# Kernel tuning notes

Measured on AMD Instinct MI355X. Metric: run time of the kernel, lower is better.

## Reference

```python
import jax, jax.numpy as jnp
from jax import lax
import numpy as np

B, L, IN_DIM = 1, 2048, 1024
D_MODEL, D_INNER, D_STATE, DT_RANK, D_CONV, N_LAYERS = 512, 1024, 16, 32, 4, 2


def _ln(x, w, b):
    m = jnp.mean(x, -1, keepdims=True)
    v = jnp.var(x, -1, keepdims=True)
    return (x - m) * lax.rsqrt(v + 1e-5) * w + b


def _rms(x, w):
    return x * lax.rsqrt(jnp.mean(x * x, -1, keepdims=True) + 1e-5) * w


def _assoc_scan(dA, dBx):
    # first-order linear recurrence h_t = dA_t * h_{t-1} + dBx_t via associative scan
    def comb(e1, e2):
        a1, b1 = e1
        a2, b2 = e2
        return a1 * a2, a2 * b1 + b2
    return lax.associative_scan(comb, (dA, dBx), axis=1)[1]


def _mamba_layer(h, in_w, cw, cb, xw, dtw, dtb, alog, Dp, ow, rw):
    hn = _rms(h, rw)                              # pre-norm (RMSNorm)
    xz = hn @ in_w                                # [b,l,2*d_inner]
    xi, z = jnp.split(xz, 2, -1)
    # causal depthwise conv1d (kernel d_conv, left pad d_conv-1)
    xc = lax.conv_general_dilated(xi.transpose(0, 2, 1), cw, (1,), [(D_CONV - 1, 0)],
                                  feature_group_count=D_INNER,
                                  dimension_numbers=('NCH', 'OIH', 'NCH')) + cb[None, :, None]
    xi = jax.nn.silu(xc.transpose(0, 2, 1))       # [b,l,d_inner]
    dbc = xi @ xw                                 # [b,l,dt_rank+2*d_state]
    dt, Bm, Cm = jnp.split(dbc, [DT_RANK, DT_RANK + D_STATE], -1)
    delta = jax.nn.softplus(dt @ dtw + dtb)       # [b,l,d_inner]
    A = -jnp.exp(alog)                            # [d_inner, d_state]
    dA = jnp.exp(delta[..., None] * A)            # [b,l,d_inner,d_state]
    dBx = (delta * xi)[..., None] * Bm[:, :, None, :]
    hs = _assoc_scan(dA, dBx)                     # [b,l,d_inner,d_state]
    y = jnp.einsum('bldn,bln->bld', hs, Cm) + xi * Dp
    y = y * jax.nn.silu(z)
    return h + y @ ow


def _conv_t(x, w, b, s, p):
    # PyTorch ConvTranspose2d, weight layout [Cin, Cout, k, k]
    kT = jnp.flip(w, (2, 3)).transpose(1, 0, 2, 3)
    pad = w.shape[2] - 1 - p
    y = lax.conv_general_dilated(x, kT, (1, 1), [(pad, pad), (pad, pad)],
                                 lhs_dilation=(s, s),
                                 dimension_numbers=('NCHW', 'OIHW', 'NCHW'))
    return y + b[None, :, None, None]


def _fwd(x, coords, W_fc1, b_fc1, W_pos, b_pos,
         mamba_in_w, mamba_conv_w, mamba_conv_b, mamba_x_w, mamba_dt_w, mamba_dt_b,
         mamba_A_log, mamba_D, mamba_out_w, mamba_rms_w,
         ln_w, ln_b, Wa1, ba1, Wa2, ba2,
         ct1_w, ct1_b, ct2_w, ct2_b, ct3_w, ct3_b, ct4_w, ct4_b, ct5_w, ct5_b):
    h = jax.nn.gelu(x @ W_fc1 + b_fc1, approximate=False)   # _fc1
    h = h + (coords @ W_pos + b_pos)[None]                  # linear pos-emb
    for l in range(N_LAYERS):
        h = _mamba_layer(h, mamba_in_w[l], mamba_conv_w[l], mamba_conv_b[l],
                         mamba_x_w[l], mamba_dt_w[l], mamba_dt_b[l],
                         mamba_A_log[l], mamba_D[l], mamba_out_w[l], mamba_rms_w[l])
    h = _ln(h, ln_w, ln_b)
    A = jnp.tanh(h @ Wa1 + ba1) @ Wa2 + ba2                 # [1,L,1]
    A = jax.nn.softmax(A.transpose(0, 2, 1), axis=-1)       # [1,1,L]
    pooled = jnp.einsum('bol,bld->bod', A, h)               # [1,1,512]
    feat = pooled.reshape(x.shape[0], D_MODEL, 1, 1)
    y = jax.nn.relu(_conv_t(feat, ct1_w, ct1_b, 1, 0))      # 1 -> 4
    y = jax.nn.relu(_conv_t(y, ct2_w, ct2_b, 4, 0))         # 4 -> 16
    y = jax.nn.relu(_conv_t(y, ct3_w, ct3_b, 2, 1))         # 16 -> 32
    y = jax.nn.relu(_conv_t(y, ct4_w, ct4_b, 2, 1))         # 32 -> 64
    return _conv_t(y, ct5_w, ct5_b, 2, 1)                   # 64 -> 128, 11 classes


def setup_inputs() -> dict:
    key = jax.random.key(0)
    ks = jax.random.split(key, 32)
    n = lambda k, s, sc=0.02: jax.random.normal(k, s, jnp.float32) * sc
    inp = {
        'x': jax.random.normal(ks[0], (B, L, IN_DIM), jnp.float32),
        'coords': jax.random.uniform(ks[1], (L, 2), jnp.float32),
        'W_fc1': n(ks[2], (IN_DIM, D_MODEL)), 'b_fc1': jnp.zeros((D_MODEL,)),
        'W_pos': n(ks[3], (2, D_MODEL)), 'b_pos': jnp.zeros((D_MODEL,)),
        'mamba_in_w': n(ks[4], (N_LAYERS, D_MODEL, 2 * D_INNER)),
        'mamba_conv_w': n(ks[5], (N_LAYERS, D_INNER, 1, D_CONV), 0.1),
        'mamba_conv_b': jnp.zeros((N_LAYERS, D_INNER)),
        'mamba_x_w': n(ks[6], (N_LAYERS, D_INNER, DT_RANK + 2 * D_STATE)),
        'mamba_dt_w': n(ks[7], (N_LAYERS, DT_RANK, D_INNER), 0.1),
        'mamba_dt_b': jnp.full((N_LAYERS, D_INNER), -4.0, jnp.float32),
        'mamba_A_log': jnp.tile(jnp.log(jnp.arange(1, D_STATE + 1, dtype=jnp.float32)), (N_LAYERS, D_INNER, 1)),
        'mamba_D': jnp.ones((N_LAYERS, D_INNER), jnp.float32),
        'mamba_out_w': n(ks[8], (N_LAYERS, D_INNER, D_MODEL)),
        'mamba_rms_w': jnp.ones((N_LAYERS, D_MODEL), jnp.float32),
        'ln_w': jnp.ones((D_MODEL,)), 'ln_b': jnp.zeros((D_MODEL,)),
        'Wa1': n(ks[9], (D_MODEL, 128)), 'ba1': jnp.zeros((128,)),
        'Wa2': n(ks[10], (128, 1)), 'ba2': jnp.zeros((1,)),
        'ct1_w': n(ks[11], (512, 256, 4, 4)), 'ct1_b': jnp.zeros((256,)),
        'ct2_w': n(ks[12], (256, 128, 4, 4)), 'ct2_b': jnp.zeros((128,)),
        'ct3_w': n(ks[13], (128, 64, 4, 4)), 'ct3_b': jnp.zeros((64,)),
        'ct4_w': n(ks[14], (64, 32, 4, 4)), 'ct4_b': jnp.zeros((32,)),
        'ct5_w': n(ks[15], (32, 11, 4, 4)), 'ct5_b': jnp.zeros((11,)),
    }
    return inp


def reference(x, coords, W_fc1, b_fc1, W_pos, b_pos,
              mamba_in_w, mamba_conv_w, mamba_conv_b, mamba_x_w, mamba_dt_w, mamba_dt_b,
              mamba_A_log, mamba_D, mamba_out_w, mamba_rms_w,
              ln_w, ln_b, Wa1, ba1, Wa2, ba2,
              ct1_w, ct1_b, ct2_w, ct2_b, ct3_w, ct3_b, ct4_w, ct4_b, ct5_w, ct5_b):
    return _fwd(x, coords, W_fc1, b_fc1, W_pos, b_pos,
                mamba_in_w, mamba_conv_w, mamba_conv_b, mamba_x_w, mamba_dt_w, mamba_dt_b,
                mamba_A_log, mamba_D, mamba_out_w, mamba_rms_w,
                ln_w, ln_b, Wa1, ba1, Wa2, ba2,
                ct1_w, ct1_b, ct2_w, ct2_b, ct3_w, ct3_b, ct4_w, ct4_b, ct5_w, ct5_b)
```

## Files before the change

### kernel.cpp

```cpp
#include <hip/hip_runtime.h>
#include <math.h>

#define LSEQ 2048
#define DM 512
#define DI 1024
#define NST 16
#define CHUNK 128
#define NC (LSEQ / CHUNK)

__device__ __forceinline__ float siluf(float v) { return v / (1.f + expf(-v)); }

__global__ __launch_bounds__(256) void gemm_mt(
    const float* __restrict__ A, int lda,
    const float* __restrict__ B, int ldb,
    float* __restrict__ out, int ldc, int Ktot)
{
    __shared__ float As[16][68];
    __shared__ float Bs[16][132];
    const int tid = threadIdx.x;
    const int tx = tid & 15, ty = tid >> 4;
    const int n0 = blockIdx.x << 7, m0 = blockIdx.y << 6;
    const int z = blockIdx.z, nz = gridDim.z;
    const int Kz = Ktot / nz, kb = z * Kz;
    const int arow = tid >> 2, ak = (tid & 3) << 2;
    const int bkr = tid >> 5, bcol = (tid & 31) << 2;
    const float* Ap = A + (size_t)(m0 + arow) * lda + kb + ak;
    const float* Bp = B + (size_t)(kb + bkr) * ldb + n0 + bcol;
    float acc[4][8] = {};
    float4 av = *(const float4*)(Ap);
    float4 bv0 = *(const float4*)(Bp);
    float4 bv1 = *(const float4*)(Bp + (size_t)8 * ldb);
    for (int k0 = 0; k0 < Kz; k0 += 16) {
        As[ak + 0][arow] = av.x;
        As[ak + 1][arow] = av.y;
        As[ak + 2][arow] = av.z;
        As[ak + 3][arow] = av.w;
        *(float4*)&Bs[bkr][bcol] = bv0;
        *(float4*)&Bs[bkr + 8][bcol] = bv1;
        __syncthreads();
        if (k0 + 16 < Kz) {
            av = *(const float4*)(Ap + k0 + 16);
            bv0 = *(const float4*)(Bp + (size_t)(k0 + 16) * ldb);
            bv1 = *(const float4*)(Bp + (size_t)(k0 + 24) * ldb);
        }
#pragma unroll
        for (int kk = 0; kk < 16; ++kk) {
            float4 a = *(const float4*)&As[kk][ty << 2];
            float4 b0 = *(const float4*)&Bs[kk][tx << 2];
            float4 b1 = *(const float4*)&Bs[kk][(tx << 2) + 64];
            float a4[4] = {a.x, a.y, a.z, a.w};
            float b8[8] = {b0.x, b0.y, b0.z, b0.w, b1.x, b1.y, b1.z, b1.w};
#pragma unroll
            for (int i = 0; i < 4; ++i)
#pragma unroll
                for (int j = 0; j < 8; ++j)
                    acc[i][j] = fmaf(a4[i], b8[j], acc[i][j]);
        }
        __syncthreads();
    }
    const int Mtot = gridDim.y << 6;
    float* op = out + (size_t)z * Mtot * ldc;
#pragma unroll
    for (int i = 0; i < 4; ++i) {
        float* Cp = op + (size_t)(m0 + (ty << 2) + i) * ldc + n0 + (tx << 2);
        *(float4*)Cp = make_float4(acc[i][0], acc[i][1], acc[i][2], acc[i][3]);
        *(float4*)(Cp + 64) = make_float4(acc[i][4], acc[i][5], acc[i][6], acc[i][7]);
    }
}

__global__ __launch_bounds__(256) void sk_reduce(
    const float* __restrict__ part, float* __restrict__ out, int S, int nz, int add)
{
    const int idx = blockIdx.x * 256 + threadIdx.x;
    if (idx >= S) return;
    float s = 0.f;
    for (int zz = 0; zz < nz; ++zz) s += part[(size_t)zz * S + idx];
    if (add) out[idx] += s; else out[idx] = s;
}

__global__ __launch_bounds__(256) void gemm64(
    const float* __restrict__ A, int lda,
    const float* __restrict__ B, int ldb,
    float* __restrict__ C, int ldc,
    int K, int accum)
{
    __shared__ float As[16][68];
    __shared__ float Bs[16][68];
    const int tid = threadIdx.x;
    const int tx = tid & 15, ty = tid >> 4;
    const int m0 = blockIdx.y << 6, n0 = blockIdx.x << 6;
    const int arow = tid >> 2, akk = (tid & 3) << 2;
    const int bkr = tid >> 4, bnn = (tid & 15) << 2;
    const float* Ap = A + (size_t)(m0 + arow) * lda + akk;
    const float* Bp = B + (size_t)bkr * ldb + n0 + bnn;
    float acc[4][4] = {};
    for (int k0 = 0; k0 < K; k0 += 16) {
        float4 av = *(const float4*)(Ap + k0);
        float4 bv = *(const float4*)(Bp + (size_t)k0 * ldb);
        As[akk + 0][arow] = av.x;
        As[akk + 1][arow] = av.y;
        As[akk + 2][arow] = av.z;
        As[akk + 3][arow] = av.w;
        *(float4*)&Bs[bkr][bnn] = bv;
        __syncthreads();
#pragma unroll
        for (int kk = 0; kk < 16; ++kk) {
            float4 a = *(const float4*)&As[kk][ty << 2];
            float4 b = *(const float4*)&Bs[kk][tx << 2];
            acc[0][0] = fmaf(a.x, b.x, acc[0][0]);
            acc[0][1] = fmaf(a.x, b.y, acc[0][1]);
            acc[0][2] = fmaf(a.x, b.z, acc[0][2]);
            acc[0][3] = fmaf(a.x, b.w, acc[0][3]);
            acc[1][0] = fmaf(a.y, b.x, acc[1][0]);
            acc[1][1] = fmaf(a.y, b.y, acc[1][1]);
            acc[1][2] = fmaf(a.y, b.z, acc[1][2]);
            acc[1][3] = fmaf(a.y, b.w, acc[1][3]);
            acc[2][0] = fmaf(a.z, b.x, acc[2][0]);
            acc[2][1] = fmaf(a.z, b.y, acc[2][1]);
            acc[2][2] = fmaf(a.z, b.z, acc[2][2]);
            acc[2][3] = fmaf(a.z, b.w, acc[2][3]);
            acc[3][0] = fmaf(a.w, b.x, acc[3][0]);
            acc[3][1] = fmaf(a.w, b.y, acc[3][1]);
            acc[3][2] = fmaf(a.w, b.z, acc[3][2]);
            acc[3][3] = fmaf(a.w, b.w, acc[3][3]);
        }
        __syncthreads();
    }
#pragma unroll
    for (int i = 0; i < 4; ++i) {
        float* Cp = C + (size_t)(m0 + (ty << 2) + i) * ldc + n0 + (tx << 2);
        if (accum) {
            Cp[0] += acc[i][0]; Cp[1] += acc[i][1]; Cp[2] += acc[i][2]; Cp[3] += acc[i][3];
        } else {
            Cp[0] = acc[i][0]; Cp[1] = acc[i][1]; Cp[2] = acc[i][2]; Cp[3] = acc[i][3];
        }
    }
}

__global__ __launch_bounds__(256) void xproj_splitk(
    const float* __restrict__ A, const float* __restrict__ B,
    float* __restrict__ part)
{
    __shared__ float As[16][68];
    __shared__ float Bs[16][68];
    const int tid = threadIdx.x;
    const int tx = tid & 15, ty = tid >> 4;
    const int ks = blockIdx.x;
    const int m0 = blockIdx.y << 6;
    const int arow = tid >> 2, ak = (tid & 3) << 2;
    const int bkr = tid >> 4, bcol = (tid & 15) << 2;
    const int kbase = ks << 7;
    const float* Ap = A + (size_t)(m0 + arow) * DI + kbase + ak;
    const float* Bp = B + (size_t)(kbase + bkr) * 64 + bcol;
    float acc[4][4] = {};
    for (int k0 = 0; k0 < 128; k0 += 16) {
        float4 av = *(const float4*)(Ap + k0);
        float4 bv = *(const float4*)(Bp + k0 * 64);
        As[ak + 0][arow] = av.x;
        As[ak + 1][arow] = av.y;
        As[ak + 2][arow] = av.z;
        As[ak + 3][arow] = av.w;
        *(float4*)&Bs[bkr][bcol] = bv;
        __syncthreads();
#pragma unroll
        for (int kk = 0; kk < 16; ++kk) {
            float4 a = *(const float4*)&As[kk][ty << 2];
            float4 b = *(const float4*)&Bs[kk][tx << 2];
            acc[0][0] = fmaf(a.x, b.x, acc[0][0]);
            acc[0][1] = fmaf(a.x, b.y, acc[0][1]);
            acc[0][2] = fmaf(a.x, b.z, acc[0][2]);
            acc[0][3] = fmaf(a.x, b.w, acc[0][3]);
            acc[1][0] = fmaf(a.y, b.x, acc[1][0]);
            acc[1][1] = fmaf(a.y, b.y, acc[1][1]);
            acc[1][2] = fmaf(a.y, b.z, acc[1][2]);
            acc[1][3] = fmaf(a.y, b.w, acc[1][3]);
            acc[2][0] = fmaf(a.z, b.x, acc[2][0]);
            acc[2][1] = fmaf(a.z, b.y, acc[2][1]);
            acc[2][2] = fmaf(a.z, b.z, acc[2][2]);
            acc[2][3] = fmaf(a.z, b.w, acc[2][3]);
            acc[3][0] = fmaf(a.w, b.x, acc[3][0]);
            acc[3][1] = fmaf(a.w, b.y, acc[3][1]);
            acc[3][2] = fmaf(a.w, b.z, acc[3][2]);
            acc[3][3] = fmaf(a.w, b.w, acc[3][3]);
        }
        __syncthreads();
    }
#pragma unroll
    for (int i = 0; i < 4; ++i) {
        float* Cp = part + ((size_t)ks * LSEQ + m0 + (ty << 2) + i) * 64 + (tx << 2);
        Cp[0] = acc[i][0]; Cp[1] = acc[i][1]; Cp[2] = acc[i][2]; Cp[3] = acc[i][3];
    }
}

__global__ __launch_bounds__(256) void xproj_reduce(
    const float* __restrict__ part, float* __restrict__ dbc)
{
    const int idx = blockIdx.x * 256 + threadIdx.x;
    float s = 0.f;
#pragma unroll
    for (int ks = 0; ks < 8; ++ks) s += part[(size_t)ks * LSEQ * 64 + idx];
    dbc[idx] = s;
}

__global__ __launch_bounds__(256) void fc1_epi(
    const float* __restrict__ tmp, const float* __restrict__ bfc1,
    const float* __restrict__ coords, const float* __restrict__ Wpos,
    const float* __restrict__ bpos, float* __restrict__ h)
{
    int idx = blockIdx.x * 256 + threadIdx.x;
    int t = idx >> 9, j = idx & 511;
    float v = tmp[idx] + bfc1[j];
    float g = 0.5f * v * (1.f + erff(v * 0.70710678118654752f));
    h[idx] = g + coords[2 * t] * Wpos[j] + coords[2 * t + 1] * Wpos[DM + j] + bpos[j];
}

__global__ __launch_bounds__(256) void rmsnorm_k(
    const float* __restrict__ h, const float* __restrict__ w, float* __restrict__ out)
{
    const int t = blockIdx.x, tid = threadIdx.x;
    float a = h[(size_t)t * DM + tid];
    float b = h[(size_t)t * DM + 256 + tid];
    float ss = a * a + b * b;
#pragma unroll
    for (int off = 1; off < 64; off <<= 1) ss += __shfl_xor(ss, off);
    __shared__ float red[4];
    if ((tid & 63) == 0) red[tid >> 6] = ss;
    __syncthreads();
    float tot = red[0] + red[1] + red[2] + red[3];
    float inv = rsqrtf(tot * (1.f / DM) + 1e-5f);
    out[(size_t)t * DM + tid] = a * inv * w[tid];
    out[(size_t)t * DM + 256 + tid] = b * inv * w[256 + tid];
}

__global__ __launch_bounds__(256) void layernorm_k(
    const float* __restrict__ h, const float* __restrict__ w,
    const float* __restrict__ bb, float* __restrict__ out)
{
    const int t = blockIdx.x, tid = threadIdx.x;
    float a = h[(size_t)t * DM + tid];
    float b = h[(size_t)t * DM + 256 + tid];
    float s = a + b;
#pragma unroll
    for (int off = 1; off < 64; off <<= 1) s += __shfl_xor(s, off);
    __shared__ float red1[4];
    if ((tid & 63) == 0) red1[tid >> 6] = s;
    __syncthreads();
    float mean = (red1[0] + red1[1] + red1[2] + red1[3]) * (1.f / DM);
    float da = a - mean, db = b - mean;
    float vs = da * da + db * db;
#pragma unroll
    for (int off = 1; off < 64; off <<= 1) vs += __shfl_xor(vs, off);
    __shared__ float red2[4];
    if ((tid & 63) == 0) red2[tid >> 6] = vs;
    __syncthreads();
    float var = (red2[0] + red2[1] + red2[2] + red2[3]) * (1.f / DM);
    float inv = rsqrtf(var + 1e-5f);
    out[(size_t)t * DM + tid] = da * inv * w[tid] + bb[tid];
    out[(size_t)t * DM + 256 + tid] = db * inv * w[256 + tid] + bb[256 + tid];
}

__global__ __launch_bounds__(256) void conv_silu_k(
    const float* __restrict__ xz, const float* __restrict__ cw,
    const float* __restrict__ cb, float* __restrict__ xc)
{
    int idx = blockIdx.x * 256 + threadIdx.x;
    int t = idx >> 10, c = idx & 1023;
    float w0 = cw[c * 4], w1 = cw[c * 4 + 1], w2 = cw[c * 4 + 2], w3 = cw[c * 4 + 3];
    float s = cb[c];
    if (t >= 3) s = fmaf(xz[(size_t)(t - 3) * 2048 + c], w0, s);
    if (t >= 2) s = fmaf(xz[(size_t)(t - 2) * 2048 + c], w1, s);
    if (t >= 1) s = fmaf(xz[(size_t)(t - 1) * 2048 + c], w2, s);
    s = fmaf(xz[(size_t)t * 2048 + c], w3, s);
    xc[idx] = siluf(s);
}

__global__ __launch_bounds__(256) void softplus_k(
    float* __restrict__ delta, const float* __restrict__ dtb)
{
    int idx = blockIdx.x * 256 + threadIdx.x;
    int d = idx & 1023;
    float v = delta[idx] + dtb[d];
    delta[idx] = fmaxf(v, 0.f) + log1pf(expf(-fabsf(v)));
}

__global__ __launch_bounds__(256) void scan_p1(
    const float* __restrict__ delta, const float* __restrict__ xc,
    const float* __restrict__ dbc, const float* __restrict__ alog,
    float* __restrict__ aprod, float* __restrict__ hfin)
{
    __shared__ float sD[CHUNK][16], sX[CHUNK][16], sB[CHUNK][16];
    const int tid = threadIdx.x;
    const int g = tid >> 4, n = tid & 15;
    const int d0 = blockIdx.x << 4;
    const int c = blockIdx.y;
    const int t0 = c * CHUNK;
    const int d = d0 + g;
    const float An = -expf(alog[d * NST + n]);
    for (int i = tid; i < CHUNK * 16; i += 256) {
        int r = i >> 4, cc = i & 15;
        sD[r][cc] = delta[(size_t)(t0 + r) * DI + d0 + cc];
        sX[r][cc] = xc[(size_t)(t0 + r) * DI + d0 + cc];
        sB[r][cc] = dbc[(size_t)(t0 + r) * 64 + 32 + cc];
    }
    __syncthreads();
    float h = 0.f, ap = 1.f;
    for (int i = 0; i < CHUNK; ++i) {
        float dl = sD[i][g], xv = sX[i][g];
        float a = expf(dl * An);
        h = fmaf(a, h, dl * xv * sB[i][n]);
        ap *= a;
    }
    size_t idx = ((size_t)c * DI + d) * NST + n;
    aprod[idx] = ap;
    hfin[idx] = h;
}

__global__ __launch_bounds__(256) void scan_carry(
    const float* __restrict__ aprod, const float* __restrict__ hfin,
    float* __restrict__ carry)
{
    const int dn = blockIdx.x * 256 + threadIdx.x;
    float h = 0.f;
    carry[dn] = 0.f;
#pragma unroll
    for (int c = 0; c < NC - 1; ++c) {
        h = fmaf(aprod[(size_t)c * DI * NST + dn], h, hfin[(size_t)c * DI * NST + dn]);
        carry[(size_t)(c + 1) * DI * NST + dn] = h;
    }
}

__global__ __launch_bounds__(256) void scan_p2(
    const float* __restrict__ delta, const float* __restrict__ xc,
    const float* __restrict__ dbc, const float* __restrict__ xz,
    const float* __restrict__ alog, const float* __restrict__ Dp,
    const float* __restrict__ carry, float* __restrict__ y)
{
    __shared__ float sD[CHUNK][16], sX[CHUNK][16], sB[CHUNK][16], sC[CHUNK][16], sZ[CHUNK][16];
    const int tid = threadIdx.x;
    const int g = tid >> 4, n = tid & 15;
    const int d0 = blockIdx.x << 4;
    const int c = blockIdx.y;
    const int t0 = c * CHUNK;
    const int d = d0 + g;
    const float An = -expf(alog[d * NST + n]);
    const float Dd = Dp[d];
    for (int i = tid; i < CHUNK * 16; i += 256) {
        int r = i >> 4, cc = i & 15;
        sD[r][cc] = delta[(size_t)(t0 + r) * DI + d0 + cc];
        sX[r][cc] = xc[(size_t)(t0 + r) * DI + d0 + cc];
        sB[r][cc] = dbc[(size_t)(t0 + r) * 64 + 32 + cc];
        sC[r][cc] = dbc[(size_t)(t0 + r) * 64 + 48 + cc];
        sZ[r][cc] = xz[(size_t)(t0 + r) * 2048 + 1024 + d0 + cc];
    }
    __syncthreads();
    float h = carry[((size_t)c * DI + d) * NST + n];
    for (int i = 0; i < CHUNK; ++i) {
        float dl = sD[i][g], xv = sX[i][g];
        float a = expf(dl * An);
        h = fmaf(a, h, dl * xv * sB[i][n]);
        float p = h * sC[i][n];
        p += __shfl_xor(p, 1, 16);
        p += __shfl_xor(p, 2, 16);
        p += __shfl_xor(p, 4, 16);
        p += __shfl_xor(p, 8, 16);
        if (n == 0) {
            float yv = p + xv * Dd;
            float zz = sZ[i][g];
            y[(size_t)(t0 + i) * DI + d] = yv * siluf(zz);
        }
    }
}

__global__ __launch_bounds__(256) void attn_fin(
    const float* __restrict__ amx, const float* __restrict__ ba1,
    const float* __restrict__ Wa2, const float* __restrict__ ba2,
    float* __restrict__ scores)
{
    const int tid = threadIdx.x;
    const int row = blockIdx.x * 4 + (tid >> 6);
    const int lane = tid & 63;
    float v = tanhf(amx[(size_t)row * 128 + lane] + ba1[lane]) * Wa2[lane]
            + tanhf(amx[(size_t)row * 128 + 64 + lane] + ba1[64 + lane]) * Wa2[64 + lane];
#pragma unroll
    for (int off = 1; off < 64; off <<= 1) v += __shfl_xor(v, off);
    if (lane == 0) scores[row] = v + ba2[0];
}

__global__ __launch_bounds__(1024) void softmax_k(
    const float* __restrict__ s, float* __restrict__ w)
{
    const int tid = threadIdx.x;
    __shared__ float red[16];
    float m = fmaxf(s[tid], s[tid + 1024]);
#pragma unroll
    for (int off = 1; off < 64; off <<= 1) m = fmaxf(m, __shfl_xor(m, off));
    if ((tid & 63) == 0) red[tid >> 6] = m;
    __syncthreads();
    if (tid < 64) {
        float mm = (tid < 16) ? red[tid] : -1e30f;
#pragma unroll
        for (int off = 1; off < 16; off <<= 1) mm = fmaxf(mm, __shfl_xor(mm, off));
        if (tid == 0) red[0] = mm;
    }
    __syncthreads();
    const float gm = red[0];
    __syncthreads();
    float e0 = expf(s[tid] - gm), e1 = expf(s[tid + 1024] - gm);
    float sum = e0 + e1;
#pragma unroll
    for (int off = 1; off < 64; off <<= 1) sum += __shfl_xor(sum, off);
    __shared__ float red2[16];
    if ((tid & 63) == 0) red2[tid >> 6] = sum;
    __syncthreads();
    if (tid < 64) {
        float ss = (tid < 16) ? red2[tid] : 0.f;
#pragma unroll
        for (int off = 1; off < 16; off <<= 1) ss += __shfl_xor(ss, off);
        if (tid == 0) red2[0] = ss;
    }
    __syncthreads();
    float inv = 1.f / red2[0];
    w[tid] = e0 * inv;
    w[tid + 1024] = e1 * inv;
}

__global__ __launch_bounds__(256) void pooled_p1(
    const float* __restrict__ wts, const float* __restrict__ hf, float* __restrict__ part)
{
    const int j = blockIdx.x * 256 + threadIdx.x;
    const int tc = blockIdx.y;
    float acc = 0.f;
    const int t0 = tc * 128;
    for (int t = t0; t < t0 + 128; ++t) acc = fmaf(wts[t], hf[(size_t)t * DM + j], acc);
    part[(size_t)tc * DM + j] = acc;
}

__global__ __launch_bounds__(256) void pooled_p2(
    const float* __restrict__ part, float* __restrict__ pooled)
{
    const int j = blockIdx.x * 256 + threadIdx.x;
    float acc = 0.f;
#pragma unroll
    for (int tc = 0; tc < 16; ++tc) acc += part[(size_t)tc * DM + j];
    pooled[j] = acc;
}

__global__ __launch_bounds__(256) void ct1_fast(
    const float* __restrict__ feat, const float* __restrict__ w,
    const float* __restrict__ b, float* __restrict__ out)
{
    __shared__ float sf[512];
    __shared__ float sRed[256];
    const int o = blockIdx.x, tid = threadIdx.x;
    sf[tid] = feat[tid];
    sf[tid + 256] = feat[tid + 256];
    __syncthreads();
    const int p = tid & 15, g = tid >> 4;
    float acc = 0.f;
#pragma unroll 8
    for (int ci = g * 32; ci < g * 32 + 32; ++ci)
        acc = fmaf(sf[ci], w[ci * 4096 + (o << 4) + p], acc);
    sRed[tid] = acc;
    __syncthreads();
    if (g == 0) {
        float s = b[o];
#pragma unroll
        for (int gg = 0; gg < 16; ++gg) s += sRed[gg * 16 + p];
        out[(o << 4) + p] = fmaxf(s, 0.f);
    }
}

__global__ __launch_bounds__(256) void ct2_fast(
    const float* __restrict__ in, const float* __restrict__ w,
    const float* __restrict__ b, float* __restrict__ out)
{
    __shared__ float sI[1024];
    __shared__ float sW[1024];
    __shared__ float sRed[256];
    const int yy = blockIdx.x, o = blockIdx.y, tid = threadIdx.x;
    const int iy = yy >> 2, ky = yy & 3;
    for (int i = tid; i < 1024; i += 256) {
        int ci = i >> 2, q = i & 3;
        sI[i] = in[(ci << 4) + (iy << 2) + q];
        sW[i] = w[ci * 2048 + (o << 4) + (ky << 2) + q];
    }
    __syncthreads();
    const int xx = tid & 15, g = tid >> 4;
    const int ix = xx >> 2, kx = xx & 3;
    float acc = 0.f;
#pragma unroll 8
    for (int ci = g * 16; ci < g * 16 + 16; ++ci)
        acc = fmaf(sI[(ci << 2) + ix], sW[(ci << 2) + kx], acc);
    sRed[tid] = acc;
    __syncthreads();
    if (g == 0) {
        float s = b[o];
#pragma unroll
        for (int gg = 0; gg < 16; ++gg) s += sRed[gg * 16 + xx];
        out[(o << 8) + (yy << 4) + xx] = fmaxf(s, 0.f);
    }
}

__global__ __launch_bounds__(256) void ctup_fast(
    const float* __restrict__ in, const float* __restrict__ w,
    const float* __restrict__ b, float* __restrict__ out,
    int Cin, int Cout, int Hin, int hshift, int relu)
{
    __shared__ float sIn[4608];
    __shared__ float sW[2048];
    __shared__ float sRed[256];
    const int tid = threadIdx.x;
    const int yy = blockIdx.x, o = blockIdx.y;
    const int Hout = Hin << 1;
    const int ST = Hin + 2;
    const int houtshift = hshift + 1;

    const int ky0 = (yy + 1) & 1;
    const int iy0 = (yy + 1 - ky0) >> 1;
    const int iy1 = iy0 - 1;
    const int row_elems = Cin * ST;

    for (int i = tid; i < 2 * row_elems; i += 256) sIn[i] = 0.f;
    __syncthreads();
    const int nload = Cin << hshift;
    if (iy0 < Hin) {
        const float* src = in + ((size_t)iy0 << hshift);
        for (int i = tid; i < nload; i += 256) {
            int ci = i >> hshift, col = i & (Hin - 1);
            sIn[ci * ST + 1 + col] = src[((size_t)ci << (2 * hshift)) + col];
        }
    }
    if (iy1 >= 0) {
        const float* src = in + ((size_t)iy1 << hshift);
        for (int i = tid; i < nload; i += 256) {
            int ci = i >> hshift, col = i & (Hin - 1);
            sIn[row_elems + ci * ST + 1 + col] = src[((size_t)ci << (2 * hshift)) + col];
        }
    }
    for (int i = tid; i < (Cin << 4); i += 256)
        sW[i] = w[(size_t)(i >> 4) * (Cout << 4) + (o << 4) + (i & 15)];
    __syncthreads();

    const int xx = tid & (Hout - 1);
    const int g = tid >> houtshift;
    const int kx0 = (xx + 1) & 1;
    const int ix0 = (xx + 1 - kx0) >> 1;
    const int k00 = (ky0 << 2) + kx0;

    float acc = 0.f;
    const float* in1 = sIn + row_elems;
#pragma unroll 4
    for (int ci = g * 16; ci < g * 16 + 16; ++ci) {
        const int base = ci * ST + ix0;
        const float* wr = &sW[ci << 4];
        float i00 = sIn[base + 1], i01 = sIn[base];
        float i10 = in1[base + 1], i11 = in1[base];
        acc = fmaf(i00, wr[k00], acc);
        acc = fmaf(i01, wr[k00 + 2], acc);
        acc = fmaf(i10, wr[k00 + 8], acc);
        acc = fmaf(i11, wr[k00 + 10], acc);
    }
    sRed[tid] = acc;
    __syncthreads();
    if (g == 0) {
        float s = b[o];
        const int XG = 256 >> houtshift;
        for (int gg = 0; gg < XG; ++gg) s += sRed[(gg << houtshift) + xx];
        out[(size_t)o * Hout * Hout + (size_t)yy * Hout + xx] = relu ? fmaxf(s, 0.f) : s;
    }
}

extern "C" void kernel_launch(void* const* d_in, const int* in_sizes, int n_in,
                              void* d_out, int out_size, void* d_ws, size_t ws_size,
                              hipStream_t stream)
{
    const float* x      = (const float*)d_in[0];
    const float* coords = (const float*)d_in[1];
    const float* Wfc1   = (const float*)d_in[2];
    const float* bfc1   = (const float*)d_in[3];
    const float* Wpos   = (const float*)d_in[4];
    const float* bpos   = (const float*)d_in[5];
    const float* in_w   = (const float*)d_in[6];
    const float* conv_w = (const float*)d_in[7];
    const float* conv_b = (const float*)d_in[8];
    const float* x_w    = (const float*)d_in[9];
    const float* dt_w   = (const float*)d_in[10];
    const float* dt_b   = (const float*)d_in[11];
    const float* A_log  = (const float*)d_in[12];
    const float* Dp     = (const float*)d_in[13];
    const float* out_w  = (const float*)d_in[14];
    const float* rms_w  = (const float*)d_in[15];
    const float* ln_w   = (const float*)d_in[16];
    const float* ln_b   = (const float*)d_in[17];
    const float* Wa1    = (const float*)d_in[18];
    const float* ba1    = (const float*)d_in[19];
    const float* Wa2    = (const float*)d_in[20];
    const float* ba2    = (const float*)d_in[21];
    const float* ct1w   = (const float*)d_in[22];
    const float* ct1b   = (const float*)d_in[23];
    const float* ct2w   = (const float*)d_in[24];
    const float* ct2b   = (const float*)d_in[25];
    const float* ct3w   = (const float*)d_in[26];
    const float* ct3b   = (const float*)d_in[27];
    const float* ct4w   = (const float*)d_in[28];
    const float* ct4b   = (const float*)d_in[29];
    const float* ct5w   = (const float*)d_in[30];
    const float* ct5b   = (const float*)d_in[31];

    float* ws     = (float*)d_ws;
    float* h      = ws;
    float* hn     = h + (size_t)LSEQ * DM;
    float* xz     = hn + (size_t)LSEQ * DM;
    float* xc     = xz + (size_t)LSEQ * 2 * DI;
    float* dbc    = xc + (size_t)LSEQ * DI;
    float* delta  = dbc + (size_t)LSEQ * 64;
    float* yb     = delta + (size_t)LSEQ * DI;
    float* hf     = yb + (size_t)LSEQ * DI;
    float* scores = hf + (size_t)LSEQ * DM;
    float* wts    = scores + LSEQ;
    float* pooled = wts + LSEQ;
    float* c1     = pooled + DM;
    float* c2     = c1 + 256 * 16;
    float* c3     = c2 + 128 * 256;
    float* c4     = c3 + 64 * 1024;
    float* aprod  = c4 + 32 * 4096;
    float* hfin   = aprod + (size_t)NC * DI * NST;
    float* carry  = hfin + (size_t)NC * DI * NST;
    float* part   = carry + (size_t)NC * DI * NST;
    float* partk  = yb;
    float* skpart = xz;
    float* amx    = xz;

    gemm_mt<<<dim3(DM / 128, LSEQ / 64, 4), 256, 0, stream>>>(x, 1024, Wfc1, DM, skpart, DM, 1024);
    sk_reduce<<<LSEQ * DM / 256, 256, 0, stream>>>(skpart, hn, LSEQ * DM, 4, 0);
    fc1_epi<<<LSEQ * DM / 256, 256, 0, stream>>>(hn, bfc1, coords, Wpos, bpos, h);

    for (int l = 0; l < 2; ++l) {
        rmsnorm_k<<<LSEQ, 256, 0, stream>>>(h, rms_w + l * DM, hn);
        gemm_mt<<<dim3(2 * DI / 128, LSEQ / 64, 1), 256, 0, stream>>>(
            hn, DM, in_w + (size_t)l * DM * 2 * DI, 2 * DI, xz, 2 * DI, DM);
        conv_silu_k<<<LSEQ * DI / 256, 256, 0, stream>>>(
            xz, conv_w + (size_t)l * DI * 4, conv_b + (size_t)l * DI, xc);
        xproj_splitk<<<dim3(8, LSEQ / 64), 256, 0, stream>>>(
            xc, x_w + (size_t)l * DI * 64, partk);
        xproj_reduce<<<LSEQ * 64 / 256, 256, 0, stream>>>(partk, dbc);
        gemm64<<<dim3(DI / 64, LSEQ / 64), 256, 0, stream>>>(
            dbc, 64, dt_w + (size_t)l * 32 * DI, DI, delta, DI, 32, 0);
        softplus_k<<<LSEQ * DI / 256, 256, 0, stream>>>(delta, dt_b + (size_t)l * DI);
        scan_p1<<<dim3(DI / 16, NC), 256, 0, stream>>>(
            delta, xc, dbc, A_log + (size_t)l * DI * NST, aprod, hfin);
        scan_carry<<<DI * NST / 256, 256, 0, stream>>>(aprod, hfin, carry);
        scan_p2<<<dim3(DI / 16, NC), 256, 0, stream>>>(
            delta, xc, dbc, xz, A_log + (size_t)l * DI * NST, Dp + (size_t)l * DI,
            carry, yb);
        gemm_mt<<<dim3(DM / 128, LSEQ / 64, 4), 256, 0, stream>>>(
            yb, DI, out_w + (size_t)l * DI * DM, DM, skpart, DM, 1024);
        sk_reduce<<<LSEQ * DM / 256, 256, 0, stream>>>(skpart, h, LSEQ * DM, 4, 1);
    }

    layernorm_k<<<LSEQ, 256, 0, stream>>>(h, ln_w, ln_b, hf);
    gemm64<<<dim3(2, LSEQ / 64), 256, 0, stream>>>(hf, DM, Wa1, 128, amx, 128, DM, 0);
    attn_fin<<<LSEQ / 4, 256, 0, stream>>>(amx, ba1, Wa2, ba2, scores);
    softmax_k<<<1, 1024, 0, stream>>>(scores, wts);
    pooled_p1<<<dim3(2, 16), 256, 0, stream>>>(wts, hf, part);
    pooled_p2<<<2, 256, 0, stream>>>(part, pooled);

    ct1_fast<<<256, 256, 0, stream>>>(pooled, ct1w, ct1b, c1);
    ct2_fast<<<dim3(16, 128), 256, 0, stream>>>(c1, ct2w, ct2b, c2);
    ctup_fast<<<dim3(32, 64), 256, 0, stream>>>(c2, ct3w, ct3b, c3, 128, 64, 16, 4, 1);
    ctup_fast<<<dim3(64, 32), 256, 0, stream>>>(c3, ct4w, ct4b, c4, 64, 32, 32, 5, 1);
    ctup_fast<<<dim3(128, 11), 256, 0, stream>>>(c4, ct5w, ct5b, (float*)d_out, 32, 11, 64, 6, 0);
}
```

Baseline: 670.2 us.

## Fuse split-K reduce with norms, fold softplus into dt GEMM, shrink GEMM tiles

Merges the split-K reduction, the fc1 GELU/pos epilogue and the following RMSNorm/LayerNorm into per-row kernels, and folds the softplus bias epilogue into a dedicated dt-projection GEMM. This removes several elementwise launches and full-tensor round trips through global memory. The main GEMM is also retiled from 64x128 tiles with 256 threads to 64x64 tiles with 128 threads, doubling the block count. That adds occupancy but lowers data reuse per block.

```diff
diff --git a/kernel.cpp b/kernel.cpp
--- a/kernel.cpp
+++ b/kernel.cpp
@@ -10,51 +10,54 @@
 
 __device__ __forceinline__ float siluf(float v) { return v / (1.f + expf(-v)); }
 
-__global__ __launch_bounds__(256) void gemm_mt(
+__global__ __launch_bounds__(128) void gemm_s(
     const float* __restrict__ A, int lda,
     const float* __restrict__ B, int ldb,
     float* __restrict__ out, int ldc, int Ktot)
 {
     __shared__ float As[16][68];
-    __shared__ float Bs[16][132];
-    const int tid = threadIdx.x;
-    const int tx = tid & 15, ty = tid >> 4;
-    const int n0 = blockIdx.x << 7, m0 = blockIdx.y << 6;
+    __shared__ float Bs[16][68];
+    const int tid = threadIdx.x;
+    const int tx = tid & 7;
+    const int ty = tid >> 3;
+    const int n0 = blockIdx.x << 6, m0 = blockIdx.y << 6;
     const int z = blockIdx.z, nz = gridDim.z;
     const int Kz = Ktot / nz, kb = z * Kz;
-    const int arow = tid >> 2, ak = (tid & 3) << 2;
-    const int bkr = tid >> 5, bcol = (tid & 31) << 2;
+    const int arow = tid >> 1, ak = (tid & 1) << 3;
+    const int bkr = tid >> 3, bcol = (tid & 7) << 3;
     const float* Ap = A + (size_t)(m0 + arow) * lda + kb + ak;
     const float* Bp = B + (size_t)(kb + bkr) * ldb + n0 + bcol;
     float acc[4][8] = {};
-    float4 av = *(const float4*)(Ap);
-    float4 bv0 = *(const float4*)(Bp);
-    float4 bv1 = *(const float4*)(Bp + (size_t)8 * ldb);
+    float4 a0 = *(const float4*)(Ap);
+    float4 a1 = *(const float4*)(Ap + 4);
+    float4 b0 = *(const float4*)(Bp);
+    float4 b1 = *(const float4*)(Bp + 4);
     for (int k0 = 0; k0 < Kz; k0 += 16) {
-        As[ak + 0][arow] = av.x;
-        As[ak + 1][arow] = av.y;
-        As[ak + 2][arow] = av.z;
-        As[ak + 3][arow] = av.w;
-        *(float4*)&Bs[bkr][bcol] = bv0;
-        *(float4*)&Bs[bkr + 8][bcol] = bv1;
+        As[ak + 0][arow] = a0.x; As[ak + 1][arow] = a0.y;
+        As[ak + 2][arow] = a0.z; As[ak + 3][arow] = a0.w;
+        As[ak + 4][arow] = a1.x; As[ak + 5][arow] = a1.y;
+        As[ak + 6][arow] = a1.z; As[ak + 7][arow] = a1.w;
+        *(float4*)&Bs[bkr][bcol] = b0;
+        *(float4*)&Bs[bkr][bcol + 4] = b1;
         __syncthreads();
         if (k0 + 16 < Kz) {
-            av = *(const float4*)(Ap + k0 + 16);
-            bv0 = *(const float4*)(Bp + (size_t)(k0 + 16) * ldb);
-            bv1 = *(const float4*)(Bp + (size_t)(k0 + 24) * ldb);
+            a0 = *(const float4*)(Ap + k0 + 16);
+            a1 = *(const float4*)(Ap + k0 + 20);
+            b0 = *(const float4*)(Bp + (size_t)(k0 + 16) * ldb);
+            b1 = *(const float4*)(Bp + (size_t)(k0 + 16) * ldb + 4);
         }
 #pragma unroll
         for (int kk = 0; kk < 16; ++kk) {
             float4 a = *(const float4*)&As[kk][ty << 2];
-            float4 b0 = *(const float4*)&Bs[kk][tx << 2];
-            float4 b1 = *(const float4*)&Bs[kk][(tx << 2) + 64];
-            float a4[4] = {a.x, a.y, a.z, a.w};
-            float b8[8] = {b0.x, b0.y, b0.z, b0.w, b1.x, b1.y, b1.z, b1.w};
+            float4 bb0 = *(const float4*)&Bs[kk][tx << 3];
+            float4 bb1 = *(const float4*)&Bs[kk][(tx << 3) + 4];
+            float av[4] = {a.x, a.y, a.z, a.w};
+            float bv[8] = {bb0.x, bb0.y, bb0.z, bb0.w, bb1.x, bb1.y, bb1.z, bb1.w};
 #pragma unroll
             for (int i = 0; i < 4; ++i)
 #pragma unroll
                 for (int j = 0; j < 8; ++j)
-                    acc[i][j] = fmaf(a4[i], b8[j], acc[i][j]);
+                    acc[i][j] = fmaf(av[i], bv[j], acc[i][j]);
         }
         __syncthreads();
     }
@@ -62,20 +65,64 @@
     float* op = out + (size_t)z * Mtot * ldc;
 #pragma unroll
     for (int i = 0; i < 4; ++i) {
-        float* Cp = op + (size_t)(m0 + (ty << 2) + i) * ldc + n0 + (tx << 2);
+        float* Cp = op + (size_t)(m0 + (ty << 2) + i) * ldc + n0 + (tx << 3);
         *(float4*)Cp = make_float4(acc[i][0], acc[i][1], acc[i][2], acc[i][3]);
-        *(float4*)(Cp + 64) = make_float4(acc[i][4], acc[i][5], acc[i][6], acc[i][7]);
-    }
-}
-
-__global__ __launch_bounds__(256) void sk_reduce(
-    const float* __restrict__ part, float* __restrict__ out, int S, int nz, int add)
-{
-    const int idx = blockIdx.x * 256 + threadIdx.x;
-    if (idx >= S) return;
-    float s = 0.f;
-    for (int zz = 0; zz < nz; ++zz) s += part[(size_t)zz * S + idx];
-    if (add) out[idx] += s; else out[idx] = s;
+        *(float4*)(Cp + 4) = make_float4(acc[i][4], acc[i][5], acc[i][6], acc[i][7]);
+    }
+}
+
+__global__ __launch_bounds__(256) void dtproj_k(
+    const float* __restrict__ A,
+    const float* __restrict__ B,
+    const float* __restrict__ dtb,
+    float* __restrict__ delta)
+{
+    __shared__ float As[16][68];
+    __shared__ float Bs[16][68];
+    const int tid = threadIdx.x;
+    const int tx = tid & 15, ty = tid >> 4;
+    const int m0 = blockIdx.y << 6, n0 = blockIdx.x << 6;
+    const int arow = tid >> 2, akk = (tid & 3) << 2;
+    const int bkr = tid >> 4, bnn = (tid & 15) << 2;
+    const float* Ap = A + (size_t)(m0 + arow) * 64 + akk;
+    const float* Bp = B + (size_t)bkr * DI + n0 + bnn;
+    float acc[4][4] = {};
+    for (int k0 = 0; k0 < 32; k0 += 16) {
+        float4 av = *(const float4*)(Ap + k0);
+        float4 bv = *(const float4*)(Bp + (size_t)k0 * DI);
+        As[akk + 0][arow] = av.x;
+        As[akk + 1][arow] = av.y;
+        As[akk + 2][arow] = av.z;
+        As[akk + 3][arow] = av.w;
+        *(float4*)&Bs[bkr][bnn] = bv;
+        __syncthreads();
+#pragma unroll
+        for (int kk = 0; kk < 16; ++kk) {
+            float4 a = *(const float4*)&As[kk][ty << 2];
+            float4 b = *(const float4*)&Bs[kk][tx << 2];
+#pragma unroll
+            for (int i = 0; i < 4; ++i) {
+                float ai = (i == 0) ? a.x : (i == 1) ? a.y : (i == 2) ? a.z : a.w;
+                acc[i][0] = fmaf(ai, b.x, acc[i][0]);
+                acc[i][1] = fmaf(ai, b.y, acc[i][1]);
+                acc[i][2] = fmaf(ai, b.z, acc[i][2]);
+                acc[i][3] = fmaf(ai, b.w, acc[i][3]);
+            }
+        }
+        __syncthreads();
+    }
+    const int col = n0 + (tx << 2);
+    float4 bb = *(const float4*)&dtb[col];
+    float bias[4] = {bb.x, bb.y, bb.z, bb.w};
+#pragma unroll
+    for (int i = 0; i < 4; ++i) {
+        float* Cp = delta + (size_t)(m0 + (ty << 2) + i) * DI + col;
+#pragma unroll
+        for (int j = 0; j < 4; ++j) {
+            float v = acc[i][j] + bias[j];
+            Cp[j] = fmaxf(v, 0.f) + log1pf(expf(-fabsf(v)));
+        }
+    }
 }
 
 __global__ __launch_bounds__(256) void gemm64(
@@ -202,61 +249,84 @@
     dbc[idx] = s;
 }
 
-__global__ __launch_bounds__(256) void fc1_epi(
-    const float* __restrict__ tmp, const float* __restrict__ bfc1,
-    const float* __restrict__ coords, const float* __restrict__ Wpos,
-    const float* __restrict__ bpos, float* __restrict__ h)
-{
-    int idx = blockIdx.x * 256 + threadIdx.x;
-    int t = idx >> 9, j = idx & 511;
-    float v = tmp[idx] + bfc1[j];
-    float g = 0.5f * v * (1.f + erff(v * 0.70710678118654752f));
-    h[idx] = g + coords[2 * t] * Wpos[j] + coords[2 * t + 1] * Wpos[DM + j] + bpos[j];
-}
-
-__global__ __launch_bounds__(256) void rmsnorm_k(
-    const float* __restrict__ h, const float* __restrict__ w, float* __restrict__ out)
+__global__ __launch_bounds__(256) void fc1_fin(
+    const float* __restrict__ part,
+    const float* __restrict__ bfc1, const float* __restrict__ coords,
+    const float* __restrict__ Wpos, const float* __restrict__ bpos,
+    const float* __restrict__ rw,
+    float* __restrict__ h, float* __restrict__ hn)
 {
     const int t = blockIdx.x, tid = threadIdx.x;
-    float a = h[(size_t)t * DM + tid];
-    float b = h[(size_t)t * DM + 256 + tid];
-    float ss = a * a + b * b;
+    const size_t base = (size_t)t * DM;
+    float va = 0.f, vb = 0.f;
+#pragma unroll
+    for (int z = 0; z < 4; ++z) {
+        va += part[(size_t)z * LSEQ * DM + base + tid];
+        vb += part[(size_t)z * LSEQ * DM + base + 256 + tid];
+    }
+    const float cx = coords[2 * t], cy = coords[2 * t + 1];
+    va += bfc1[tid];
+    vb += bfc1[256 + tid];
+    float ga = 0.5f * va * (1.f + erff(va * 0.70710678118654752f));
+    float gb = 0.5f * vb * (1.f + erff(vb * 0.70710678118654752f));
+    ga += cx * Wpos[tid] + cy * Wpos[DM + tid] + bpos[tid];
+    gb += cx * Wpos[256 + tid] + cy * Wpos[DM + 256 + tid] + bpos[256 + tid];
+    h[base + tid] = ga;
+    h[base + 256 + tid] = gb;
+    float ss = ga * ga + gb * gb;
 #pragma unroll
     for (int off = 1; off < 64; off <<= 1) ss += __shfl_xor(ss, off);
     __shared__ float red[4];
     if ((tid & 63) == 0) red[tid >> 6] = ss;
     __syncthreads();
-    float tot = red[0] + red[1] + red[2] + red[3];
-    float inv = rsqrtf(tot * (1.f / DM) + 1e-5f);
-    out[(size_t)t * DM + tid] = a * inv * w[tid];
-    out[(size_t)t * DM + 256 + tid] = b * inv * w[256 + tid];
-}
-
-__global__ __launch_bounds__(256) void layernorm_k(
-    const float* __restrict__ h, const float* __restrict__ w,
-    const float* __restrict__ bb, float* __restrict__ out)
+    float inv = rsqrtf((red[0] + red[1] + red[2] + red[3]) * (1.f / DM) + 1e-5f);
+    hn[base + tid] = ga * inv * rw[tid];
+    hn[base + 256 + tid] = gb * inv * rw[256 + tid];
+}
+
+__global__ __launch_bounds__(256) void skadd_norm(
+    const float* __restrict__ part,
+    float* __restrict__ h,
+    const float* __restrict__ w1, const float* __restrict__ b1,
+    float* __restrict__ outb, int mode)
 {
     const int t = blockIdx.x, tid = threadIdx.x;
-    float a = h[(size_t)t * DM + tid];
-    float b = h[(size_t)t * DM + 256 + tid];
-    float s = a + b;
-#pragma unroll
-    for (int off = 1; off < 64; off <<= 1) s += __shfl_xor(s, off);
-    __shared__ float red1[4];
-    if ((tid & 63) == 0) red1[tid >> 6] = s;
-    __syncthreads();
-    float mean = (red1[0] + red1[1] + red1[2] + red1[3]) * (1.f / DM);
-    float da = a - mean, db = b - mean;
-    float vs = da * da + db * db;
-#pragma unroll
-    for (int off = 1; off < 64; off <<= 1) vs += __shfl_xor(vs, off);
-    __shared__ float red2[4];
-    if ((tid & 63) == 0) red2[tid >> 6] = vs;
-    __syncthreads();
-    float var = (red2[0] + red2[1] + red2[2] + red2[3]) * (1.f / DM);
-    float inv = rsqrtf(var + 1e-5f);
-    out[(size_t)t * DM + tid] = da * inv * w[tid] + bb[tid];
-    out[(size_t)t * DM + 256 + tid] = db * inv * w[256 + tid] + bb[256 + tid];
+    const size_t base = (size_t)t * DM;
+    float va = h[base + tid], vb = h[base + 256 + tid];
+#pragma unroll
+    for (int z = 0; z < 4; ++z) {
+        va += part[(size_t)z * LSEQ * DM + base + tid];
+        vb += part[(size_t)z * LSEQ * DM + base + 256 + tid];
+    }
+    h[base + tid] = va;
+    h[base + 256 + tid] = vb;
+    __shared__ float red1[4], red2[4];
+    if (mode == 0) {
+        float ss = va * va + vb * vb;
+#pragma unroll
+        for (int off = 1; off < 64; off <<= 1) ss += __shfl_xor(ss, off);
+        if ((tid & 63) == 0) red1[tid >> 6] = ss;
+        __syncthreads();
+        float inv = rsqrtf((red1[0] + red1[1] + red1[2] + red1[3]) * (1.f / DM) + 1e-5f);
+        outb[base + tid] = va * inv * w1[tid];
+        outb[base + 256 + tid] = vb * inv * w1[256 + tid];
+    } else {
+        float s = va + vb;
+#pragma unroll
+        for (int off = 1; off < 64; off <<= 1) s += __shfl_xor(s, off);
+        if ((tid & 63) == 0) red1[tid >> 6] = s;
+        __syncthreads();
+        float mean = (red1[0] + red1[1] + red1[2] + red1[3]) * (1.f / DM);
+        float da = va - mean, db = vb - mean;
+        float vs = da * da + db * db;
+#pragma unroll
+        for (int off = 1; off < 64; off <<= 1) vs += __shfl_xor(vs, off);
+        if ((tid & 63) == 0) red2[tid >> 6] = vs;
+        __syncthreads();
+        float inv = rsqrtf((red2[0] + red2[1] + red2[2] + red2[3]) * (1.f / DM) + 1e-5f);
+        outb[base + tid] = da * inv * w1[tid] + b1[tid];
+        outb[base + 256 + tid] = db * inv * w1[256 + tid] + b1[256 + tid];
+    }
 }
 
 __global__ __launch_bounds__(256) void conv_silu_k(
@@ -272,15 +342,6 @@
     if (t >= 1) s = fmaf(xz[(size_t)(t - 1) * 2048 + c], w2, s);
     s = fmaf(xz[(size_t)t * 2048 + c], w3, s);
     xc[idx] = siluf(s);
-}
-
-__global__ __launch_bounds__(256) void softplus_k(
-    float* __restrict__ delta, const float* __restrict__ dtb)
-{
-    int idx = blockIdx.x * 256 + threadIdx.x;
-    int d = idx & 1023;
-    float v = delta[idx] + dtb[d];
-    delta[idx] = fmaxf(v, 0.f) + log1pf(expf(-fabsf(v)));
 }
 
 __global__ __launch_bounds__(256) void scan_p1(
@@ -631,34 +692,33 @@
     float* skpart = xz;
     float* amx    = xz;
 
-    gemm_mt<<<dim3(DM / 128, LSEQ / 64, 4), 256, 0, stream>>>(x, 1024, Wfc1, DM, skpart, DM, 1024);
-    sk_reduce<<<LSEQ * DM / 256, 256, 0, stream>>>(skpart, hn, LSEQ * DM, 4, 0);
-    fc1_epi<<<LSEQ * DM / 256, 256, 0, stream>>>(hn, bfc1, coords, Wpos, bpos, h);
+    gemm_s<<<dim3(DM / 64, LSEQ / 64, 4), 128, 0, stream>>>(x, 1024, Wfc1, DM, skpart, DM, 1024);
+    fc1_fin<<<LSEQ, 256, 0, stream>>>(skpart, bfc1, coords, Wpos, bpos, rms_w, h, hn);
 
     for (int l = 0; l < 2; ++l) {
-        rmsnorm_k<<<LSEQ, 256, 0, stream>>>(h, rms_w + l * DM, hn);
-        gemm_mt<<<dim3(2 * DI / 128, LSEQ / 64, 1), 256, 0, stream>>>(
+        gemm_s<<<dim3(2 * DI / 64, LSEQ / 64, 1), 128, 0, stream>>>(
             hn, DM, in_w + (size_t)l * DM * 2 * DI, 2 * DI, xz, 2 * DI, DM);
         conv_silu_k<<<LSEQ * DI / 256, 256, 0, stream>>>(
             xz, conv_w + (size_t)l * DI * 4, conv_b + (size_t)l * DI, xc);
         xproj_splitk<<<dim3(8, LSEQ / 64), 256, 0, stream>>>(
             xc, x_w + (size_t)l * DI * 64, partk);
         xproj_reduce<<<LSEQ * 64 / 256, 256, 0, stream>>>(partk, dbc);
-        gemm64<<<dim3(DI / 64, LSEQ / 64), 256, 0, stream>>>(
-            dbc, 64, dt_w + (size_t)l * 32 * DI, DI, delta, DI, 32, 0);
-        softplus_k<<<LSEQ * DI / 256, 256, 0, stream>>>(delta, dt_b + (size_t)l * DI);
+        dtproj_k<<<dim3(DI / 64, LSEQ / 64), 256, 0, stream>>>(
+            dbc, dt_w + (size_t)l * 32 * DI, dt_b + (size_t)l * DI, delta);
         scan_p1<<<dim3(DI / 16, NC), 256, 0, stream>>>(
             delta, xc, dbc, A_log + (size_t)l * DI * NST, aprod, hfin);
         scan_carry<<<DI * NST / 256, 256, 0, stream>>>(aprod, hfin, carry);
         scan_p2<<<dim3(DI / 16, NC), 256, 0, stream>>>(
             delta, xc, dbc, xz, A_log + (size_t)l * DI * NST, Dp + (size_t)l * DI,
             carry, yb);
-        gemm_mt<<<dim3(DM / 128, LSEQ / 64, 4), 256, 0, stream>>>(
+        gemm_s<<<dim3(DM / 64, LSEQ / 64, 4), 128, 0, stream>>>(
             yb, DI, out_w + (size_t)l * DI * DM, DM, skpart, DM, 1024);
-        sk_reduce<<<LSEQ * DM / 256, 256, 0, stream>>>(skpart, h, LSEQ * DM, 4, 1);
-    }
-
-    layernorm_k<<<LSEQ, 256, 0, stream>>>(h, ln_w, ln_b, hf);
+        if (l == 0)
+            skadd_norm<<<LSEQ, 256, 0, stream>>>(skpart, h, rms_w + DM, nullptr, hn, 0);
+        else
+            skadd_norm<<<LSEQ, 256, 0, stream>>>(skpart, h, ln_w, ln_b, hf, 1);
+    }
+
     gemm64<<<dim3(2, LSEQ / 64), 256, 0, stream>>>(hf, DM, Wa1, 128, amx, 128, DM, 0);
     attn_fin<<<LSEQ / 4, 256, 0, stream>>>(amx, ba1, Wa2, ba2, scores);
     softmax_k<<<1, 1024, 0, stream>>>(scores, wts);
```

New measurement: 679.5 us. Within noise of the previous version (+1.4%).
